# Kernel optimization log

Measured on AMD Instinct MI355X. Metric: run time of the kernel, lower is better.

Reference implementation:

```python
import jax, jax.numpy as jnp
import numpy as np

TEMPERATURE = 2.0 / 3.0
LIMIT_A = -0.1
LIMIT_B = 1.1

N_NODES = 50000
N_CLUSTERS = 64
N_RELATIONS = 8
N_EDGES = 1000000


def setup_inputs() -> dict:
    key = jax.random.key(0)
    ks = jax.random.split(key, 6)
    xavier = float(np.sqrt(6.0 / (N_CLUSTERS + N_CLUSTERS)))
    return {
        "assignments": jax.random.normal(ks[0], (N_NODES, N_CLUSTERS), jnp.float32),
        "inter_cluster_logits": jax.random.uniform(ks[1], (N_RELATIONS, N_CLUSTERS, N_CLUSTERS), jnp.float32, -xavier, xavier),
        "log_alpha": jnp.zeros((N_RELATIONS, N_CLUSTERS, N_CLUSTERS), jnp.float32),
        "absent_bias": jnp.zeros((N_RELATIONS,), jnp.float32),
        "edge_index": jax.random.randint(ks[2], (2, N_EDGES), 0, N_NODES, jnp.int32),
        "edge_type": jax.random.randint(ks[3], (N_EDGES,), 0, N_RELATIONS, jnp.int32),
        "neg_edge_index": jax.random.randint(ks[4], (2, N_EDGES), 0, N_NODES, jnp.int32),
        "neg_edge_type": jax.random.randint(ks[5], (N_EDGES,), 0, N_RELATIONS, jnp.int32),
    }


def _edge_logits(assignments, weights, absent_bias, edge_index, edge_type):
    # src, dst: [E, C] gathers (irregular access)
    src = assignments[edge_index[0]]
    dst = assignments[edge_index[1]]
    n_rel = weights.shape[0]
    # torch.bmm(W[et], dst[:, :, None]) == dst @ W[et].T ; compute per relation
    # (fixed small relation loop; avoids materializing [E, C, C]) then select.
    logits_all = jnp.stack(
        [jnp.sum(src * (dst @ weights[r].T), axis=-1) for r in range(n_rel)],
        axis=-1,
    )  # [E, R]
    logits = jnp.take_along_axis(logits_all, edge_type[:, None], axis=1)[:, 0]
    return logits + absent_bias[edge_type]


def reference(assignments, inter_cluster_logits, log_alpha, absent_bias,
              edge_index, edge_type, neg_edge_index, neg_edge_type):
    # Hard-concrete gate, eval mode: z = clamp(sigmoid(log_alpha)*(b-a)+a, 0, 1)
    gate = jnp.clip(jax.nn.sigmoid(log_alpha) * (LIMIT_B - LIMIT_A) + LIMIT_A, 0.0, 1.0)
    weights = jax.nn.sigmoid(inter_cluster_logits) * gate  # [R, C, C]

    pos_logits = _edge_logits(assignments, weights, absent_bias, edge_index, edge_type)
    neg_logits = _edge_logits(assignments, weights, absent_bias, neg_edge_index, neg_edge_type)

    # BCE-with-logits: target=1 -> softplus(-x); target=0 -> softplus(x)
    pos_loss = jnp.mean(jax.nn.softplus(-pos_logits))
    neg_loss = jnp.mean(jax.nn.softplus(neg_logits))
    return pos_loss + neg_loss
```

## Files before the change

kernel.cpp:

```cpp
#include <hip/hip_runtime.h>
#include <hip/hip_bf16.h>
#include <math.h>

#define E_EDGES 1000000
#define N_NODES 50000
#define N_C     64
#define N_REL   8
#define CHB     1024
#define CAP     192
#define NBLK    977
#define BT      256
#define SENT    0xFFFFFFFFu

typedef __attribute__((ext_vector_type(4))) float floatx4;
typedef __attribute__((ext_vector_type(2))) float floatx2;

static __device__ __forceinline__ unsigned pk4_fp8(float a, float b, float c, float d) {
    unsigned w = 0;
    w = __builtin_amdgcn_cvt_pk_fp8_f32(a, b, w, false);
    w = __builtin_amdgcn_cvt_pk_fp8_f32(c, d, w, true);
    return w;
}

static __device__ __forceinline__ long long pack64(unsigned lo, unsigned hi) {
    uint2 u; u.x = lo; u.y = hi;
    return __builtin_bit_cast(long long, u);
}

__global__ __launch_bounds__(256) void prep_kernel(
    const float* __restrict__ assign,
    const float* __restrict__ icl,
    const float* __restrict__ la,
    unsigned char* __restrict__ Wp8,
    unsigned char* __restrict__ AS8,
    float* __restrict__ out)
{
    int tid = blockIdx.x * blockDim.x + threadIdx.x;
    int nth = gridDim.x * blockDim.x;
    if (tid == 0) out[0] = 0.0f;

    for (int idx = tid; idx < N_REL * N_C * 16; idx += nth) {
        int row = idx >> 4, dq = idx & 15;
        int q = dq >> 2, c = (dq >> 1) & 1, jh = dq & 1;
        int k0 = (2 * c + jh) * 16 + 4 * q;
        float wv[4];
        #pragma unroll
        for (int b = 0; b < 4; ++b) {
            int srci = (row << 6) + k0 + b;
            float w = 1.0f / (1.0f + __expf(-icl[srci]));
            float g = 1.0f / (1.0f + __expf(-la[srci])) * 1.2f - 0.1f;
            g = fminf(fmaxf(g, 0.0f), 1.0f);
            wv[b] = w * g;
        }
        ((unsigned*)Wp8)[idx] = pk4_fp8(wv[0], wv[1], wv[2], wv[3]);
    }

    for (int n = tid; n < N_NODES; n += nth) {
        const float4* a4 = (const float4*)(assign + (size_t)n * N_C);
        unsigned w[16];
        #pragma unroll
        for (int i = 0; i < 16; ++i) {
            float4 v = a4[i];
            w[i] = pk4_fp8(v.x, v.y, v.z, v.w);
        }
        uint4* as = (uint4*)(AS8 + (size_t)n * N_C);
        #pragma unroll
        for (int q = 0; q < 4; ++q) {
            uint4 o;
            o.x = w[0 * 4 + q];
            o.y = w[1 * 4 + q];
            o.z = w[2 * 4 + q];
            o.w = w[3 * 4 + q];
            as[q] = o;
        }
    }
}

__global__ __launch_bounds__(BT, 5) void edge_kernel(
    const unsigned char* __restrict__ AS8,
    const unsigned char* __restrict__ Wp8,
    const float* __restrict__ absent_bias,
    const int* __restrict__ ei, const int* __restrict__ et,
    const int* __restrict__ nei, const int* __restrict__ net,
    float* __restrict__ out)
{
    __shared__ unsigned list[N_REL * CAP];
    __shared__ unsigned cnt[N_REL];
    __shared__ float red[4];
    if (threadIdx.x < N_REL) cnt[threadIdx.x] = 0u;
    __syncthreads();

    int blk = blockIdx.x;
    bool isneg = blk >= NBLK;
    int lb = isneg ? blk - NBLK : blk;
    const int* Es = isneg ? nei : ei;
    const int* Et = isneg ? net : et;
    float sign = isneg ? 1.0f : -1.0f;
    int base = lb * CHB;
    int elim = min(base + CHB, E_EDGES);

    {
        int e0 = base + threadIdx.x;
        int sv[4], dv[4], rv[4];
        bool mv[4];
        #pragma unroll
        for (int k = 0; k < 4; ++k) {
            int e = e0 + k * BT;
            mv[k] = e < elim;
            int ec = mv[k] ? e : base;
            sv[k] = __builtin_nontemporal_load(&Es[ec]);
            dv[k] = __builtin_nontemporal_load(&Es[E_EDGES + ec]);
            rv[k] = __builtin_nontemporal_load(&Et[ec]);
        }
        #pragma unroll
        for (int k = 0; k < 4; ++k) {
            if (mv[k]) {
                unsigned rank = atomicAdd(&cnt[rv[k]], 1u);
                if (rank < CAP)
                    list[rv[k] * CAP + rank] = (unsigned)sv[k] | ((unsigned)dv[k] << 16);
            }
        }
    }
    __syncthreads();

    if (threadIdx.x < N_REL * 16) {
        int r = threadIdx.x >> 4;
        int i = threadIdx.x & 15;
        int n = min((int)cnt[r], CAP);
        int padded = ((n + 15) >> 4) << 4;
        int slot = n + i;
        if (slot < padded) list[r * CAP + slot] = SENT;
    }
    __syncthreads();

    int lane = threadIdx.x & 63;
    int wid  = __builtin_amdgcn_readfirstlane(threadIdx.x >> 6);
    int n16  = lane & 15;
    int quad = lane >> 4;
    float loss = 0.0f;

    int G0 = __builtin_amdgcn_readfirstlane((min((int)cnt[0], CAP) + 15) >> 4);
    int G1 = __builtin_amdgcn_readfirstlane((min((int)cnt[1], CAP) + 15) >> 4);
    int G2 = __builtin_amdgcn_readfirstlane((min((int)cnt[2], CAP) + 15) >> 4);
    int G3 = __builtin_amdgcn_readfirstlane((min((int)cnt[3], CAP) + 15) >> 4);
    int G4 = __builtin_amdgcn_readfirstlane((min((int)cnt[4], CAP) + 15) >> 4);
    int G5 = __builtin_amdgcn_readfirstlane((min((int)cnt[5], CAP) + 15) >> 4);
    int G6 = __builtin_amdgcn_readfirstlane((min((int)cnt[6], CAP) + 15) >> 4);
    int G7 = __builtin_amdgcn_readfirstlane((min((int)cnt[7], CAP) + 15) >> 4);
    int go1 = G0;
    int go2 = go1 + G1;
    int go3 = go2 + G2;
    int go4 = go3 + G3;
    int go5 = go4 + G4;
    int go6 = go5 + G5;
    int go7 = go6 + G6;
    int tg  = go7 + G7;

    #define LOCATE(ITEM, R, GOF)                                   \
        do {                                                       \
            R = 0; GOF = 0;                                        \
            if ((ITEM) >= go1) { R = 1; GOF = go1; }               \
            if ((ITEM) >= go2) { R = 2; GOF = go2; }               \
            if ((ITEM) >= go3) { R = 3; GOF = go3; }               \
            if ((ITEM) >= go4) { R = 4; GOF = go4; }               \
            if ((ITEM) >= go5) { R = 5; GOF = go5; }               \
            if ((ITEM) >= go6) { R = 6; GOF = go6; }               \
            if ((ITEM) >= go7) { R = 7; GOF = go7; }               \
        } while (0)

    #define ISSUE(VIT, RREG, RECV, SREG, DREG)                               \
        do {                                                                 \
            if ((VIT) < end) {                                               \
                int gof_;                                                    \
                LOCATE(VIT, RREG, gof_);                                     \
                RECV = list[RREG * CAP + ((VIT) - gof_) * 16 + n16];         \
                unsigned sm_ = RECV != SENT ? (RECV & 0xFFFFu) : 0u;         \
                unsigned dm_ = RECV != SENT ? (RECV >> 16) : 0u;             \
                SREG = *(const uint4*)(AS8 + ((size_t)sm_ << 6) + quad * 16);\
                DREG = *(const uint4*)(AS8 + ((size_t)dm_ << 6) + quad * 16);\
            } else {                                                         \
                RECV = SENT;                                                 \
            }                                                                \
        } while (0)

    #define RELOADW(RREG)                                                    \
        do {                                                                 \
            if ((RREG) != rW) {                                              \
                rW = (RREG);                                                 \
                _Pragma("unroll")                                            \
                for (int mt = 0; mt < 4; ++mt)                               \
                    wfm[mt] = *(const uint4*)(Wp8 +                          \
                        ((rW * 64 + mt * 16 + n16) << 6) + quad * 16);       \
                bias = absent_bias[rW];                                      \
            }                                                                \
        } while (0)

    #define COMPUTE(RECV, SS, DD)                                            \
        do {                                                                 \
            long long bD0 = pack64((DD).x, (DD).y);                          \
            long long bD1 = pack64((DD).z, (DD).w);                          \
            unsigned sw0 = (SS).x, sw1 = (SS).y, sw2 = (SS).z, sw3 = (SS).w; \
            float d0 = 0.0f, d1 = 0.0f;                                      \
            {                                                                \
                floatx4 p0 = zero4, p1 = zero4;                              \
                p0 = __builtin_amdgcn_mfma_f32_16x16x32_fp8_fp8(             \
                        pack64(wfm[0].x, wfm[0].y), bD0, p0, 0, 0, 0);       \
                p1 = __builtin_amdgcn_mfma_f32_16x16x32_fp8_fp8(             \
                        pack64(wfm[1].x, wfm[1].y), bD0, p1, 0, 0, 0);       \
                p0 = __builtin_amdgcn_mfma_f32_16x16x32_fp8_fp8(             \
                        pack64(wfm[0].z, wfm[0].w), bD1, p0, 0, 0, 0);       \
                p1 = __builtin_amdgcn_mfma_f32_16x16x32_fp8_fp8(             \
                        pack64(wfm[1].z, wfm[1].w), bD1, p1, 0, 0, 0);       \
                floatx2 lo0 = __builtin_amdgcn_cvt_pk_f32_fp8((int)sw0, false);\
                floatx2 hi0 = __builtin_amdgcn_cvt_pk_f32_fp8((int)sw0, true);\
                floatx2 lo1 = __builtin_amdgcn_cvt_pk_f32_fp8((int)sw1, false);\
                floatx2 hi1 = __builtin_amdgcn_cvt_pk_f32_fp8((int)sw1, true);\
                d0 = fmaf(lo0.x, p0[0], d0); d1 = fmaf(lo1.x, p1[0], d1);    \
                d0 = fmaf(lo0.y, p0[1], d0); d1 = fmaf(lo1.y, p1[1], d1);    \
                d0 = fmaf(hi0.x, p0[2], d0); d1 = fmaf(hi1.x, p1[2], d1);    \
                d0 = fmaf(hi0.y, p0[3], d0); d1 = fmaf(hi1.y, p1[3], d1);    \
            }                                                                \
            {                                                                \
                floatx4 p0 = zero4, p1 = zero4;                              \
                p0 = __builtin_amdgcn_mfma_f32_16x16x32_fp8_fp8(             \
                        pack64(wfm[2].x, wfm[2].y), bD0, p0, 0, 0, 0);       \
                p1 = __builtin_amdgcn_mfma_f32_16x16x32_fp8_fp8(             \
                        pack64(wfm[3].x, wfm[3].y), bD0, p1, 0, 0, 0);       \
                p0 = __builtin_amdgcn_mfma_f32_16x16x32_fp8_fp8(             \
                        pack64(wfm[2].z, wfm[2].w), bD1, p0, 0, 0, 0);       \
                p1 = __builtin_amdgcn_mfma_f32_16x16x32_fp8_fp8(             \
                        pack64(wfm[3].z, wfm[3].w), bD1, p1, 0, 0, 0);       \
                floatx2 lo0 = __builtin_amdgcn_cvt_pk_f32_fp8((int)sw2, false);\
                floatx2 hi0 = __builtin_amdgcn_cvt_pk_f32_fp8((int)sw2, true);\
                floatx2 lo1 = __builtin_amdgcn_cvt_pk_f32_fp8((int)sw3, false);\
                floatx2 hi1 = __builtin_amdgcn_cvt_pk_f32_fp8((int)sw3, true);\
                d0 = fmaf(lo0.x, p0[0], d0); d1 = fmaf(lo1.x, p1[0], d1);    \
                d0 = fmaf(lo0.y, p0[1], d0); d1 = fmaf(lo1.y, p1[1], d1);    \
                d0 = fmaf(hi0.x, p0[2], d0); d1 = fmaf(hi1.x, p1[2], d1);    \
                d0 = fmaf(hi0.y, p0[3], d0); d1 = fmaf(hi1.y, p1[3], d1);    \
            }                                                                \
            float dot = d0 + d1;                                             \
            dot += __shfl_xor(dot, 16);                                      \
            dot += __shfl_xor(dot, 32);                                      \
            float x = sign * (dot + bias);                                   \
            float sp = fmaxf(x, 0.0f) + __logf(1.0f + __expf(-fabsf(x)));    \
            bool live = (quad == 0) && (RECV != SENT);                       \
            loss += live ? sp : 0.0f;                                        \
        } while (0)

    int start = (wid * tg) >> 2;
    int end   = ((wid + 1) * tg) >> 2;

    uint4 wfm[4];
    float bias = 0.0f;
    int rW = -1;
    const floatx4 zero4 = {0.0f, 0.0f, 0.0f, 0.0f};

    if (start < end) {
        int rA = 0, rB = 0, rC = 0;
        unsigned recA, recB, recC;
        uint4 SA = {0,0,0,0}, DA = {0,0,0,0};
        uint4 SB = {0,0,0,0}, DB = {0,0,0,0};
        uint4 SC = {0,0,0,0}, DC = {0,0,0,0};

        int vA = start, vB = start + 1, vC = start + 2;
        ISSUE(vA, rA, recA, SA, DA);
        ISSUE(vB, rB, recB, SB, DB);
        ISSUE(vC, rC, recC, SC, DC);
        RELOADW(rA);

        int n3 = (end - start + 2) / 3;
        #pragma clang loop unroll(disable)
        for (int k = 0; k < n3; ++k) {
            COMPUTE(recA, SA, DA);
            vA += 3;
            int rAn = rA;
            ISSUE(vA, rAn, recA, SA, DA);
            RELOADW(rB);

            COMPUTE(recB, SB, DB);
            vB += 3;
            int rBn = rB;
            ISSUE(vB, rBn, recB, SB, DB);
            RELOADW(rC);

            COMPUTE(recC, SC, DC);
            vC += 3;
            int rCn = rC;
            ISSUE(vC, rCn, recC, SC, DC);
            rA = rAn; rB = rBn; rC = rCn;
            RELOADW(rA);
        }
    }

    loss += __shfl_xor(loss, 1);
    loss += __shfl_xor(loss, 2);
    loss += __shfl_xor(loss, 4);
    loss += __shfl_xor(loss, 8);
    loss += __shfl_xor(loss, 16);
    loss += __shfl_xor(loss, 32);
    if (lane == 0) red[wid] = loss;
    __syncthreads();
    if (threadIdx.x == 0) {
        float t = red[0] + red[1] + red[2] + red[3];
        atomicAdd(out, t * (1.0f / (float)E_EDGES));
    }
}

extern "C" void kernel_launch(void* const* d_in, const int* in_sizes, int n_in,
                              void* d_out, int out_size, void* d_ws, size_t ws_size,
                              hipStream_t stream) {
    const float* assign = (const float*)d_in[0];
    const float* icl    = (const float*)d_in[1];
    const float* la     = (const float*)d_in[2];
    const float* ab     = (const float*)d_in[3];
    const int*   ei     = (const int*)d_in[4];
    const int*   et     = (const int*)d_in[5];
    const int*   nei    = (const int*)d_in[6];
    const int*   net    = (const int*)d_in[7];
    float* out = (float*)d_out;

    char* basep = (char*)d_ws;
    unsigned char* Wp8 = (unsigned char*)basep;
    unsigned char* AS8 = (unsigned char*)(basep + 65536);

    prep_kernel<<<256, 256, 0, stream>>>(assign, icl, la, Wp8, AS8, out);
    edge_kernel<<<2 * NBLK, BT, 0, stream>>>(AS8, Wp8, ab, ei, et, nei, net, out);
}
```

Measured before the change: 134.4 us.

## Stage fp8 relation weights in swizzled LDS and prefetch per-slot fragments

Each block now copies all eight packed fp8 relation weight matrices (32KB) into LDS using an XOR swizzle, and caches the bias values there as well. The conditional global reload of weight fragments on relation change is gone. Instead, each of the three pipeline slots loads its own weight fragments and bias from LDS at issue time, and the loop becomes branchless by clamping the item index. This removes the serialized global weight reloads from the critical path, at the cost of extra LDS usage and more registers, so the occupancy hint drops from 5 to 4 blocks.

```diff
diff --git a/kernel.cpp b/kernel.cpp
--- a/kernel.cpp
+++ b/kernel.cpp
@@ -76,7 +76,7 @@
     }
 }
 
-__global__ __launch_bounds__(BT, 5) void edge_kernel(
+__global__ __launch_bounds__(BT, 4) void edge_kernel(
     const unsigned char* __restrict__ AS8,
     const unsigned char* __restrict__ Wp8,
     const float* __restrict__ absent_bias,
@@ -84,11 +84,24 @@
     const int* __restrict__ nei, const int* __restrict__ net,
     float* __restrict__ out)
 {
+    __shared__ uint4 Wl4[N_REL * N_C * 4];
     __shared__ unsigned list[N_REL * CAP];
+    __shared__ float bias_l[N_REL];
     __shared__ unsigned cnt[N_REL];
     __shared__ float red[4];
-    if (threadIdx.x < N_REL) cnt[threadIdx.x] = 0u;
-    __syncthreads();
+    if (threadIdx.x < N_REL) {
+        cnt[threadIdx.x] = 0u;
+        bias_l[threadIdx.x] = absent_bias[threadIdx.x];
+    }
+
+    {
+        const uint4* Wg = (const uint4*)Wp8;
+        #pragma unroll
+        for (int k = 0; k < 8; ++k) {
+            int e = threadIdx.x + k * BT;
+            Wl4[e ^ ((e >> 2) & 7)] = Wg[e];
+        }
+    }
 
     int blk = blockIdx.x;
     bool isneg = blk >= NBLK;
@@ -98,6 +111,8 @@
     float sign = isneg ? 1.0f : -1.0f;
     int base = lb * CHB;
     int elim = min(base + CHB, E_EDGES);
+
+    __syncthreads();
 
     {
         int e0 = base + threadIdx.x;
@@ -155,6 +170,7 @@
     int go6 = go5 + G5;
     int go7 = go6 + G6;
     int tg  = go7 + G7;
+    int tgm1 = tg - 1;
 
     #define LOCATE(ITEM, R, GOF)                                   \
         do {                                                       \
@@ -168,34 +184,32 @@
             if ((ITEM) >= go7) { R = 7; GOF = go7; }               \
         } while (0)
 
-    #define ISSUE(VIT, RREG, RECV, SREG, DREG)                               \
+    #define ISSUE(VIT, RECV, SREG, DREG, WF0, WF1, WF2, WF3, BI)             \
         do {                                                                 \
-            if ((VIT) < end) {                                               \
-                int gof_;                                                    \
-                LOCATE(VIT, RREG, gof_);                                     \
-                RECV = list[RREG * CAP + ((VIT) - gof_) * 16 + n16];         \
-                unsigned sm_ = RECV != SENT ? (RECV & 0xFFFFu) : 0u;         \
-                unsigned dm_ = RECV != SENT ? (RECV >> 16) : 0u;             \
-                SREG = *(const uint4*)(AS8 + ((size_t)sm_ << 6) + quad * 16);\
-                DREG = *(const uint4*)(AS8 + ((size_t)dm_ << 6) + quad * 16);\
-            } else {                                                         \
-                RECV = SENT;                                                 \
+            int vc_ = (VIT) < tgm1 ? (VIT) : tgm1;                           \
+            int r_, gof_;                                                    \
+            LOCATE(vc_, r_, gof_);                                           \
+            unsigned recr_ = list[r_ * CAP + (vc_ - gof_) * 16 + n16];       \
+            RECV = (VIT) < end ? recr_ : SENT;                               \
+            unsigned sm_ = RECV != SENT ? (RECV & 0xFFFFu) : 0u;             \
+            unsigned dm_ = RECV != SENT ? (RECV >> 16) : 0u;                 \
+            SREG = *(const uint4*)(AS8 + ((size_t)sm_ << 6) + quad * 16);    \
+            DREG = *(const uint4*)(AS8 + ((size_t)dm_ << 6) + quad * 16);    \
+            int rb_ = r_ * 64 + n16;                                         \
+            {                                                                \
+                int row0_ = rb_;                                             \
+                WF0 = Wl4[(row0_ * 4 + quad) ^ (row0_ & 7)];                 \
+                int row1_ = rb_ + 16;                                        \
+                WF1 = Wl4[(row1_ * 4 + quad) ^ (row1_ & 7)];                 \
+                int row2_ = rb_ + 32;                                        \
+                WF2 = Wl4[(row2_ * 4 + quad) ^ (row2_ & 7)];                 \
+                int row3_ = rb_ + 48;                                        \
+                WF3 = Wl4[(row3_ * 4 + quad) ^ (row3_ & 7)];                 \
             }                                                                \
+            BI = bias_l[r_];                                                 \
         } while (0)
 
-    #define RELOADW(RREG)                                                    \
-        do {                                                                 \
-            if ((RREG) != rW) {                                              \
-                rW = (RREG);                                                 \
-                _Pragma("unroll")                                            \
-                for (int mt = 0; mt < 4; ++mt)                               \
-                    wfm[mt] = *(const uint4*)(Wp8 +                          \
-                        ((rW * 64 + mt * 16 + n16) << 6) + quad * 16);       \
-                bias = absent_bias[rW];                                      \
-            }                                                                \
-        } while (0)
-
-    #define COMPUTE(RECV, SS, DD)                                            \
+    #define COMPUTE(RECV, SS, DD, WF0, WF1, WF2, WF3, BI)                    \
         do {                                                                 \
             long long bD0 = pack64((DD).x, (DD).y);                          \
             long long bD1 = pack64((DD).z, (DD).w);                          \
@@ -204,13 +218,13 @@
             {                                                                \
                 floatx4 p0 = zero4, p1 = zero4;                              \
                 p0 = __builtin_amdgcn_mfma_f32_16x16x32_fp8_fp8(             \
-                        pack64(wfm[0].x, wfm[0].y), bD0, p0, 0, 0, 0);       \
+                        pack64((WF0).x, (WF0).y), bD0, p0, 0, 0, 0);         \
                 p1 = __builtin_amdgcn_mfma_f32_16x16x32_fp8_fp8(             \
-                        pack64(wfm[1].x, wfm[1].y), bD0, p1, 0, 0, 0);       \
+                        pack64((WF1).x, (WF1).y), bD0, p1, 0, 0, 0);         \
                 p0 = __builtin_amdgcn_mfma_f32_16x16x32_fp8_fp8(             \
-                        pack64(wfm[0].z, wfm[0].w), bD1, p0, 0, 0, 0);       \
+                        pack64((WF0).z, (WF0).w), bD1, p0, 0, 0, 0);         \
                 p1 = __builtin_amdgcn_mfma_f32_16x16x32_fp8_fp8(             \
-                        pack64(wfm[1].z, wfm[1].w), bD1, p1, 0, 0, 0);       \
+                        pack64((WF1).z, (WF1).w), bD1, p1, 0, 0, 0);         \
                 floatx2 lo0 = __builtin_amdgcn_cvt_pk_f32_fp8((int)sw0, false);\
                 floatx2 hi0 = __builtin_amdgcn_cvt_pk_f32_fp8((int)sw0, true);\
                 floatx2 lo1 = __builtin_amdgcn_cvt_pk_f32_fp8((int)sw1, false);\
@@ -223,13 +237,13 @@
             {                                                                \
                 floatx4 p0 = zero4, p1 = zero4;                              \
                 p0 = __builtin_amdgcn_mfma_f32_16x16x32_fp8_fp8(             \
-                        pack64(wfm[2].x, wfm[2].y), bD0, p0, 0, 0, 0);       \
+                        pack64((WF2).x, (WF2).y), bD0, p0, 0, 0, 0);         \
                 p1 = __builtin_amdgcn_mfma_f32_16x16x32_fp8_fp8(             \
-                        pack64(wfm[3].x, wfm[3].y), bD0, p1, 0, 0, 0);       \
+                        pack64((WF3).x, (WF3).y), bD0, p1, 0, 0, 0);         \
                 p0 = __builtin_amdgcn_mfma_f32_16x16x32_fp8_fp8(             \
-                        pack64(wfm[2].z, wfm[2].w), bD1, p0, 0, 0, 0);       \
+                        pack64((WF2).z, (WF2).w), bD1, p0, 0, 0, 0);         \
                 p1 = __builtin_amdgcn_mfma_f32_16x16x32_fp8_fp8(             \
-                        pack64(wfm[3].z, wfm[3].w), bD1, p1, 0, 0, 0);       \
+                        pack64((WF3).z, (WF3).w), bD1, p1, 0, 0, 0);         \
                 floatx2 lo0 = __builtin_amdgcn_cvt_pk_f32_fp8((int)sw2, false);\
                 floatx2 hi0 = __builtin_amdgcn_cvt_pk_f32_fp8((int)sw2, true);\
                 floatx2 lo1 = __builtin_amdgcn_cvt_pk_f32_fp8((int)sw3, false);\
@@ -242,7 +256,7 @@
             float dot = d0 + d1;                                             \
             dot += __shfl_xor(dot, 16);                                      \
             dot += __shfl_xor(dot, 32);                                      \
-            float x = sign * (dot + bias);                                   \
+            float x = sign * (dot + (BI));                                   \
             float sp = fmaxf(x, 0.0f) + __logf(1.0f + __expf(-fabsf(x)));    \
             bool live = (quad == 0) && (RECV != SENT);                       \
             loss += live ? sp : 0.0f;                                        \
@@ -251,45 +265,33 @@
     int start = (wid * tg) >> 2;
     int end   = ((wid + 1) * tg) >> 2;
 
-    uint4 wfm[4];
-    float bias = 0.0f;
-    int rW = -1;
     const floatx4 zero4 = {0.0f, 0.0f, 0.0f, 0.0f};
 
     if (start < end) {
-        int rA = 0, rB = 0, rC = 0;
         unsigned recA, recB, recC;
-        uint4 SA = {0,0,0,0}, DA = {0,0,0,0};
-        uint4 SB = {0,0,0,0}, DB = {0,0,0,0};
-        uint4 SC = {0,0,0,0}, DC = {0,0,0,0};
+        uint4 SA, DA, SB, DB, SC, DC;
+        uint4 wA0, wA1, wA2, wA3, wB0, wB1, wB2, wB3, wC0, wC1, wC2, wC3;
+        float bA, bB, bC;
 
         int vA = start, vB = start + 1, vC = start + 2;
-        ISSUE(vA, rA, recA, SA, DA);
-        ISSUE(vB, rB, recB, SB, DB);
-        ISSUE(vC, rC, recC, SC, DC);
-        RELOADW(rA);
+        ISSUE(vA, recA, SA, DA, wA0, wA1, wA2, wA3, bA);
+        ISSUE(vB, recB, SB, DB, wB0, wB1, wB2, wB3, bB);
+        ISSUE(vC, recC, SC, DC, wC0, wC1, wC2, wC3, bC);
 
         int n3 = (end - start + 2) / 3;
         #pragma clang loop unroll(disable)
         for (int k = 0; k < n3; ++k) {
-            COMPUTE(recA, SA, DA);
+            COMPUTE(recA, SA, DA, wA0, wA1, wA2, wA3, bA);
             vA += 3;
-            int rAn = rA;
-            ISSUE(vA, rAn, recA, SA, DA);
-            RELOADW(rB);
-
-            COMPUTE(recB, SB, DB);
+            ISSUE(vA, recA, SA, DA, wA0, wA1, wA2, wA3, bA);
+
+            COMPUTE(recB, SB, DB, wB0, wB1, wB2, wB3, bB);
             vB += 3;
-            int rBn = rB;
-            ISSUE(vB, rBn, recB, SB, DB);
-            RELOADW(rC);
-
-            COMPUTE(recC, SC, DC);
+            ISSUE(vB, recB, SB, DB, wB0, wB1, wB2, wB3, bB);
+
+            COMPUTE(recC, SC, DC, wC0, wC1, wC2, wC3, bC);
             vC += 3;
-            int rCn = rC;
-            ISSUE(vC, rCn, recC, SC, DC);
-            rA = rAn; rB = rBn; rC = rCn;
-            RELOADW(rA);
+            ISSUE(vC, recC, SC, DC, wC0, wC1, wC2, wC3, bC);
         }
     }
 
```

Result: slower. 137.1 us (+2.0%).
